# Optimization experiments

Measured on AMD Instinct MI355X. Metric: run time of the kernel, lower is better.

The kernel has to match this reference:

```python
import jax, jax.numpy as jnp
import numpy as np

B, T, V, EMB, KBD, H, NF, OUT = 256, 50, 100000, 64, 64, 128, 10, 64


def setup_inputs() -> dict:
    key = jax.random.key(0)
    ks = jax.random.split(key, 18)
    s = 0.05
    f = lambda i, shape: jax.random.normal(ks[i], shape, jnp.float32) * s
    return {
        "X": jax.random.randint(ks[0], (B, T), 0, V),
        "E": f(1, (V, EMB)),
        "KBE": f(2, (V, KBD)),
        "r_matrix": f(3, (NF, KBD)),
        "gru_Wih": f(4, (3 * H, EMB)),
        "gru_Whh": f(5, (3 * H, H)),
        "gru_bih": f(6, (3 * H,)),
        "gru_bhh": f(7, (3 * H,)),
        "u_W": f(8, (KBD, H)),
        "u_b": f(9, (KBD,)),
        "ea_W": f(10, (KBD, KBD)),
        "ea_b": f(11, (KBD,)),
        "u2_W": f(12, (H, KBD + H)),
        "u2_b": f(13, (H,)),
        "m1_W": f(14, (OUT, H)),
        "m1_b": f(15, (OUT,)),
        "m2_W": f(16, (OUT, EMB + KBD)),
        "m2_b": f(17, (OUT,)),
    }


def reference(X, E, KBE, r_matrix, gru_Wih, gru_Whh, gru_bih, gru_bhh,
              u_W, u_b, ea_W, ea_b, u2_W, u2_b, m1_W, m1_b, m2_W, m2_b):
    b, t = X.shape
    nf, d = r_matrix.shape
    hdim = gru_Whh.shape[1]
    # mask row 0 of the embedding tables (padding item)
    Em = E.at[0].set(0.0)
    KBEm = KBE.at[0].set(0.0)
    Sx = Em[X]        # [B,T,EMB]
    KBx = KBEm[X]     # [B,T,KBD]

    h0 = jnp.zeros((b, hdim), Sx.dtype)
    MN0 = jnp.zeros((b, nf, d), Sx.dtype)
    ysum0 = jnp.zeros((b, m1_b.shape[0]), Sx.dtype)

    def step(carry, xs):
        h, MN, ysum = carry
        x_emb, kb = xs
        # torch GRUCell
        gi = x_emb @ gru_Wih.T + gru_bih
        gh = h @ gru_Whh.T + gru_bhh
        ir, iz, inn = jnp.split(gi, 3, axis=1)
        hr, hz, hn = jnp.split(gh, 3, axis=1)
        r = jax.nn.sigmoid(ir + hr)
        z = jax.nn.sigmoid(iz + hz)
        n = jnp.tanh(inn + r * hn)
        h = (1.0 - z) * n + z * h
        # memory write
        EA = jnp.tanh(kb @ ea_W.T + ea_b)[:, None, :] + r_matrix      # [B,NF,D]
        gate = jax.nn.sigmoid(jnp.sum(MN * EA, axis=-1, keepdims=True))  # [B,NF,1]
        MN = MN * (1.0 - gate) + EA * gate
        # memory read
        U = jnp.tanh(h @ u_W.T + u_b)                                  # [B,D]
        AW = jax.nn.softmax(U @ r_matrix.T, axis=1)                    # [B,NF]
        AC = jnp.einsum('bnd,bn->bd', MN, AW)                          # [B,D]
        Ut = jnp.tanh(jnp.concatenate([h, AC], axis=-1) @ u2_W.T + u2_b)
        y = jnp.tanh(Ut @ m1_W.T + m1_b)                               # [B,OUT]
        return (h, MN, ysum + y), None

    (h, MN, ysum), _ = jax.lax.scan(
        step, (h0, MN0, ysum0),
        (Sx.transpose(1, 0, 2), KBx.transpose(1, 0, 2)))
    y = ysum / t

    MergeE = jnp.concatenate([E, KBE], axis=1).at[0].set(0.0)  # [V, EMB+KBD]
    Sy = jnp.tanh(MergeE @ m2_W.T + m2_b)                      # [V, OUT]
    return jax.nn.log_softmax(y @ Sy.T, axis=1)                # [B, V]
```

## Files before the change

kernel.cpp:

```cpp
#include <hip/hip_runtime.h>
#include <hip/hip_bf16.h>
#include <math.h>

#define BB 256
#define TT 50
#define VV 100000
#define EMB 64
#define KBD 64
#define HH 128
#define NF 10
#define OUTD 64
#define G3H 384
#define NTILE 6250
#define DSTR 16
#define NSY 240
#define TCH 4
#define NUTY (16*13)

typedef __attribute__((ext_vector_type(8))) short sh8;
typedef __attribute__((ext_vector_type(4))) short sh4;
typedef __attribute__((ext_vector_type(4))) float f32x4;

__device__ __forceinline__ float frcp(float x){ return __builtin_amdgcn_rcpf(x); }
__device__ __forceinline__ float sigm(float x){ return frcp(1.0f+__expf(-x)); }
__device__ __forceinline__ float tanhf_(float x){ return 1.0f - 2.0f*frcp(__expf(2.0f*x)+1.0f); }
__device__ __forceinline__ short f2bs(float f){ __hip_bfloat16 h=__float2bfloat16(f); return *reinterpret_cast<short*>(&h); }
__device__ __forceinline__ sh8 ldfrag(const float* p){
  float4 a = *(const float4*)p; float4 b = *(const float4*)(p+4);
  sh8 v;
  v[0]=f2bs(a.x); v[1]=f2bs(a.y); v[2]=f2bs(a.z); v[3]=f2bs(a.w);
  v[4]=f2bs(b.x); v[5]=f2bs(b.y); v[6]=f2bs(b.z); v[7]=f2bs(b.w);
  return v;
}
__device__ __forceinline__ sh8 ldfrag_s(const float* p, float s){
  float4 a = *(const float4*)p; float4 b = *(const float4*)(p+4);
  sh8 v;
  v[0]=f2bs(a.x*s); v[1]=f2bs(a.y*s); v[2]=f2bs(a.z*s); v[3]=f2bs(a.w*s);
  v[4]=f2bs(b.x*s); v[5]=f2bs(b.y*s); v[6]=f2bs(b.z*s); v[7]=f2bs(b.w*s);
  return v;
}
__device__ __forceinline__ void barrier_lds(){
  asm volatile("s_waitcnt lgkmcnt(0)" ::: "memory");
  __builtin_amdgcn_sched_barrier(0);
  __builtin_amdgcn_s_barrier();
  __builtin_amdgcn_sched_barrier(0);
}

#define PREP 32
__global__ __launch_bounds__(512) void k_pre(
    const int* __restrict__ X, const float* __restrict__ E, const float* __restrict__ KBE,
    const float* __restrict__ Wih, const float* __restrict__ bih, const float* __restrict__ bhh,
    const float* __restrict__ eaW, const float* __restrict__ eab,
    float* __restrict__ gi_pre, float* __restrict__ ea_pre,
    __hip_bfloat16* __restrict__ ea_bfT, float* __restrict__ denom,
    float* __restrict__ ybf32,
    const float* __restrict__ m2W, const float* __restrict__ m2b,
    __hip_bfloat16* __restrict__ Sy) {
  const int tid = threadIdx.x;
  const int w = tid>>6, l = tid&63, r16 = l&15, g4 = l>>4;

  if (blockIdx.x >= 400) {
    int kof = g4*8;
    sh8 bbf[4][4];
    float bias[4];
    #pragma unroll
    for (int nt=0;nt<4;nt++){
      int o = nt*16 + r16;
      bias[nt] = m2b[o];
      #pragma unroll
      for (int ks=0;ks<4;ks++) bbf[nt][ks] = ldfrag(m2W + o*128 + ks*32 + kof);
    }
    int wid = (blockIdx.x-400)*8 + w;
    for (int tile=wid; tile<NTILE; tile+=NSY*8){
      int v = tile*16 + r16;
      sh8 aa[4];
      const float* ep = E + (size_t)v*EMB + kof;
      const float* kp = KBE + (size_t)v*KBD + kof;
      aa[0] = ldfrag(ep); aa[1] = ldfrag(ep+32);
      aa[2] = ldfrag(kp); aa[3] = ldfrag(kp+32);
      if (v==0){ sh8 z={0,0,0,0,0,0,0,0}; aa[0]=z;aa[1]=z;aa[2]=z;aa[3]=z; }
      f32x4 acc[4];
      #pragma unroll
      for (int nt=0;nt<4;nt++){ f32x4 z={0.f,0.f,0.f,0.f}; acc[nt]=z; }
      #pragma unroll
      for (int nt=0;nt<4;nt++)
        #pragma unroll
        for (int ks=0;ks<4;ks++)
          acc[nt] = __builtin_amdgcn_mfma_f32_16x16x32_bf16(aa[ks],bbf[nt][ks],acc[nt],0,0,0);
      #pragma unroll
      for (int nt=0;nt<4;nt++){
        #pragma unroll
        for (int r=0;r<4;r++){
          int vv = tile*16 + g4*4 + r;
          Sy[(size_t)vv*OUTD + nt*16 + r16] = __float2bfloat16(tanhf_(acc[nt][r] + bias[nt]));
        }
      }
    }
    return;
  }

  if (blockIdx.x == 0){
    for (int i=tid;i<BB*DSTR;i+=512) denom[i]=0.f;
    for (int i=tid;i<BB*OUTD;i+=512) ybf32[i]=0.f;
  }
  __shared__ float xeL[PREP][68];
  __shared__ float kbL[PREP][68];
  int base = blockIdx.x * PREP;
  for (int i=tid; i<PREP*EMB; i+=512){
    int p=i>>6, k=i&63; int x = X[base+p];
    xeL[p][k] = x ? E[(size_t)x*EMB+k] : 0.0f;
    kbL[p][k] = x ? KBE[(size_t)x*KBD+k] : 0.0f;
  }
  __syncthreads();

  const int m = w>>2, nq = w&3;
  sh8 axe[2], akb[2];
  #pragma unroll
  for (int f=0;f<2;f++){
    axe[f] = ldfrag(&xeL[m*16 + r16][f*32 + g4*8]);
    akb[f] = ldfrag(&kbL[m*16 + r16][f*32 + g4*8]);
  }
  #pragma unroll
  for (int i=0;i<6;i++){
    int nt = nq*6 + i;
    int j = nt*16 + r16;
    sh8 bf0 = ldfrag(Wih + (size_t)j*EMB + g4*8);
    sh8 bf1 = ldfrag(Wih + (size_t)j*EMB + 32 + g4*8);
    f32x4 acc = {0.f,0.f,0.f,0.f};
    acc = __builtin_amdgcn_mfma_f32_16x16x32_bf16(axe[0], bf0, acc,0,0,0);
    acc = __builtin_amdgcn_mfma_f32_16x16x32_bf16(axe[1], bf1, acc,0,0,0);
    float bj = bih[j] + (j < 2*HH ? bhh[j] : 0.0f);
    #pragma unroll
    for (int r=0;r<4;r++){
      int pair = base + m*16 + g4*4 + r;
      gi_pre[(size_t)pair*G3H + j] = acc[r] + bj;
    }
  }
  {
    int d = nq*16 + r16;
    sh8 bf0 = ldfrag(eaW + (size_t)d*KBD + g4*8);
    sh8 bf1 = ldfrag(eaW + (size_t)d*KBD + 32 + g4*8);
    f32x4 acc = {0.f,0.f,0.f,0.f};
    acc = __builtin_amdgcn_mfma_f32_16x16x32_bf16(akb[0], bf0, acc,0,0,0);
    acc = __builtin_amdgcn_mfma_f32_16x16x32_bf16(akb[1], bf1, acc,0,0,0);
    float bd = eab[d];
    #pragma unroll
    for (int r=0;r<4;r++){
      int pair = base + m*16 + g4*4 + r;
      float v = tanhf(acc[r] + bd);
      ea_pre[(size_t)pair*KBD + d] = v;
      int bb = pair/TT, tt = pair - bb*TT;
      ea_bfT[((size_t)bb*64 + d)*64 + tt] = __float2bfloat16(v);
    }
  }
}

__global__ __launch_bounds__(256,2) void k_scanh(
    const float* __restrict__ gi_pre,
    const float* __restrict__ Whh, const float* __restrict__ bhh,
    const float* __restrict__ ea_pre, const float* __restrict__ rmat,
    float* __restrict__ Gg, float* __restrict__ Pg,
    __hip_bfloat16* __restrict__ h_stream) {
  const int tid = threadIdx.x;
  const int w = tid>>6, l = tid&63, r16 = l&15, g4 = l>>4;

  if (blockIdx.x >= 16) {
    const int b = (blockIdx.x-16)*4 + w;
    sh8 aa[4][2];
    #pragma unroll
    for (int i=0;i<4;i++){
      int row = i*16 + r16; if (row > TT-1) row = TT-1;
      #pragma unroll
      for (int f=0;f<2;f++)
        aa[i][f] = ldfrag(ea_pre + ((size_t)b*TT + row)*KBD + f*32 + g4*8);
    }
    sh8 rmB[2];
    #pragma unroll
    for (int f=0;f<2;f++){
      sh8 z = {0,0,0,0,0,0,0,0};
      if (r16 < NF) z = ldfrag(rmat + (size_t)r16*KBD + f*32 + g4*8);
      rmB[f] = z;
    }
    float* Gb = Gg + ((size_t)b<<12);
    #pragma unroll
    for (int i=0;i<4;i++){
      #pragma unroll
      for (int j=0;j<4;j++){
        f32x4 acc={0.f,0.f,0.f,0.f};
        #pragma unroll
        for (int f=0;f<2;f++) acc = __builtin_amdgcn_mfma_f32_16x16x32_bf16(aa[i][f], aa[j][f], acc,0,0,0);
        #pragma unroll
        for (int r=0;r<4;r++) Gb[(i*16+g4*4+r)*64 + j*16+r16] = acc[r];
      }
      f32x4 accp={0.f,0.f,0.f,0.f};
      #pragma unroll
      for (int f=0;f<2;f++) accp = __builtin_amdgcn_mfma_f32_16x16x32_bf16(aa[i][f], rmB[f], accp,0,0,0);
      #pragma unroll
      for (int r=0;r<4;r++) Pg[((size_t)b<<10) + (i*16+g4*4+r)*16 + r16] = accp[r];
    }
    return;
  }

  __shared__ __hip_bfloat16 hcat[2][16][128];
  __builtin_amdgcn_s_setprio(1);
  const int b = blockIdx.x;
  const int b0 = b*16;
  for (int i=tid;i<2*16*128;i+=256) ((short*)hcat)[i]=0;
  __syncthreads();
  const int swz = (r16&7)<<4;

  sh8 whhF[2][3][4];
  #pragma unroll
  for (int t=0;t<2;t++)
    #pragma unroll
    for (int g=0;g<3;g++){
      int chain = (w + 4*t) + 8*g;
      #pragma unroll
      for (int f=0;f<4;f++)
        whhF[t][g][f] = ldfrag(Whh + (size_t)(chain*16 + r16)*HH + f*32 + g4*8);
    }
  float4 bhn[2];
  bhn[0] = *(const float4*)(bhh + 2*HH + w*16 + g4*4);
  bhn[1] = *(const float4*)(bhh + 2*HH + (w+4)*16 + g4*4);
  float h_old[2][4] = {{0.f,0.f,0.f,0.f},{0.f,0.f,0.f,0.f}};
  const float* gi_row = gi_pre + (size_t)(b0+r16)*TT*G3H;
  __hip_bfloat16* hsb = h_stream + (size_t)b*TT*16*HH;

  int cur = 0;
  auto stepfn = [&](int s, float4 (&gi)[2][3], int cu){
    const char* hrow = (const char*)&hcat[cu][r16][0];
    sh8 hb[4];
    #pragma unroll
    for (int f=0;f<4;f++)
      hb[f] = *(const sh8*)(hrow + ((f*64 + g4*16) ^ swz));
    f32x4 aR[2], aZ[2], aN[2];
    #pragma unroll
    for (int t=0;t<2;t++){ f32x4 z={0.f,0.f,0.f,0.f}; aR[t]=z; aZ[t]=z; aN[t]=z; }
    #pragma unroll
    for (int f=0;f<4;f++){
      #pragma unroll
      for (int t=0;t<2;t++){
        aR[t] = __builtin_amdgcn_mfma_f32_16x16x32_bf16(whhF[t][0][f], hb[f], aR[t],0,0,0);
        aZ[t] = __builtin_amdgcn_mfma_f32_16x16x32_bf16(whhF[t][1][f], hb[f], aZ[t],0,0,0);
        aN[t] = __builtin_amdgcn_mfma_f32_16x16x32_bf16(whhF[t][2][f], hb[f], aN[t],0,0,0);
      }
    }
    char* hwrow = (char*)&hcat[cu^1][r16][0];
    #pragma unroll
    for (int t=0;t<2;t++){
      sh4 hp;
      #pragma unroll
      for (int r=0;r<4;r++){
        float rr = sigm(gi[t][0][r] + aR[t][r]);
        float zz = sigm(gi[t][1][r] + aZ[t][r]);
        float nn = tanhf_(gi[t][2][r] + rr*(aN[t][r] + bhn[t][r]));
        h_old[t][r] = (1.f-zz)*nn + zz*h_old[t][r];
        hp[r] = f2bs(h_old[t][r]);
      }
      *(sh4*)(hwrow + (((w+4*t)*32 + g4*8) ^ swz)) = hp;
      *(sh4*)(hsb + ((size_t)s*16 + r16)*HH + (w+4*t)*16 + g4*4) = hp;
    }
    barrier_lds();
  };

  float4 gA[2][3], gB[2][3];
  #pragma unroll
  for (int t=0;t<2;t++)
    #pragma unroll
    for (int g=0;g<3;g++)
      gA[t][g] = *(const float4*)(gi_row + g*128 + (w+4*t)*16 + g4*4);

  for (int s=0;s<TT;s+=2){
    {
      int sg = s+1;
      #pragma unroll
      for (int t=0;t<2;t++)
        #pragma unroll
        for (int g=0;g<3;g++)
          gB[t][g] = *(const float4*)(gi_row + (size_t)sg*G3H + g*128 + (w+4*t)*16 + g4*4);
      stepfn(s, gA, cur);
      cur ^= 1;
    }
    {
      int sg = (s+2<TT)? s+2 : TT-1;
      #pragma unroll
      for (int t=0;t<2;t++)
        #pragma unroll
        for (int g=0;g<3;g++)
          gA[t][g] = *(const float4*)(gi_row + (size_t)sg*G3H + g*128 + (w+4*t)*16 + g4*4);
      stepfn(s+1, gB, cur);
      cur ^= 1;
    }
  }
}

__global__ __launch_bounds__(640) void k_mnac(
    const float* __restrict__ Gg, const float* __restrict__ Pg,
    const float* __restrict__ rmat,
    const __hip_bfloat16* __restrict__ h_stream,
    const float* __restrict__ uW, const float* __restrict__ ub,
    const __hip_bfloat16* __restrict__ ea_bfT,
    __hip_bfloat16* __restrict__ ac_pre) {
  __shared__ __hip_bfloat16 U_sh[64][72];
  __shared__ float aw_sh[64*16];
  __shared__ float AagL[64*52];
  __shared__ float BagL[64*16];
  const int tid = threadIdx.x;
  const int n = tid>>6, l = tid&63, r16 = l&15, g4 = l>>4;
  const int b = blockIdx.x;
  for (int i=tid;i<64*52;i+=640) AagL[i]=0.f;
  for (int i=tid;i<64*16;i+=640) BagL[i]=0.f;

  const __hip_bfloat16* hsb = h_stream + ((size_t)(b>>4)*TT)*16*HH + (size_t)(b&15)*HH;

  #pragma unroll
  for (int cc=0; cc<2; cc++){
    int c = n + cc*10;
    if (c < 16){
      int mi = c>>2, ni = c&3;
      int t = mi*16 + r16; int tt = (t<TT)? t : TT-1;
      sh8 hfr[4], wfr[4];
      #pragma unroll
      for (int f=0;f<4;f++){
        hfr[f] = *(const sh8*)(hsb + (size_t)tt*16*HH + f*32 + g4*8);
        wfr[f] = ldfrag(uW + (size_t)(ni*16+r16)*HH + f*32 + g4*8);
      }
      f32x4 acc = {0.f,0.f,0.f,0.f};
      #pragma unroll
      for (int f=0;f<4;f++)
        acc = __builtin_amdgcn_mfma_f32_16x16x32_bf16(wfr[f], hfr[f], acc,0,0,0);
      float4 ubv = *(const float4*)(ub + ni*16 + g4*4);
      #pragma unroll
      for (int r=0;r<4;r++)
        U_sh[mi*16 + r16][ni*16 + g4*4 + r] = __float2bfloat16(tanhf_(acc[r] + ubv[r]));
    }
  }
  __syncthreads();
  if (n < 4){
    sh8 rmF[2];
    #pragma unroll
    for (int f=0;f<2;f++){
      sh8 z = {0,0,0,0,0,0,0,0};
      if (r16 < NF) z = ldfrag(rmat + (size_t)r16*KBD + f*32 + g4*8);
      rmF[f] = z;
    }
    sh8 uf[2];
    #pragma unroll
    for (int f=0;f<2;f++) uf[f] = *(const sh8*)&U_sh[n*16 + r16][f*32 + g4*8];
    f32x4 al={0.f,0.f,0.f,0.f};
    #pragma unroll
    for (int f=0;f<2;f++) al = __builtin_amdgcn_mfma_f32_16x16x32_bf16(rmF[f], uf[f], al,0,0,0);
    float mx = -1e30f;
    #pragma unroll
    for (int r=0;r<4;r++){ if (g4*4+r < NF) mx = fmaxf(mx, al[r]); }
    mx = fmaxf(mx, __shfl_xor(mx,16));
    mx = fmaxf(mx, __shfl_xor(mx,32));
    float av[4]; float ssum=0.f;
    #pragma unroll
    for (int r=0;r<4;r++){ av[r] = (g4*4+r < NF) ? __expf(al[r]-mx) : 0.f; ssum += av[r]; }
    ssum += __shfl_xor(ssum,16); ssum += __shfl_xor(ssum,32);
    float inv = frcp(ssum);
    #pragma unroll
    for (int r=0;r<4;r++){
      int nn = g4*4+r;
      if (nn < NF) aw_sh[(n*16 + r16)*16 + nn] = av[r]*inv;
    }
  }
  __syncthreads();

  float rv = rmat[n*KBD + l];
  float R = rv*rv;
  R += __shfl_xor(R,1); R += __shfl_xor(R,2); R += __shfl_xor(R,4);
  R += __shfl_xor(R,8); R += __shfl_xor(R,16); R += __shfl_xor(R,32);

  float Pn = (l<TT)? Pg[((size_t)b<<10) + l*16 + n] : 0.f;
  const float* Gb = Gg + ((size_t)b<<12);
  float Grow = Gb[l];
  float d=0.f, w_=0.f, q=1.f;

  for (int t=0;t<TT;t++){
    int tn = (t+1<TT)? t+1 : TT-1;
    float GrowN = Gb[tn*64 + l];
    float dt = __shfl(d, t);
    float g  = sigm(dt);
    float og = 1.f - g;
    float Pt = __shfl(Pn, t);
    float Ets = Grow + Pt + Pn + R;
    d = og*d + g*Ets;
    w_ = (l==t)? g : w_*og;
    q *= og;
    float awt = aw_sh[t*16 + n];
    if (l < TT) atomicAdd(&AagL[t*52 + l], awt*w_);
    if (l == 0) BagL[t*16 + n] = awt*(1.f - q);
    Grow = GrowN;
  }
  __syncthreads();

  if (n < 4){
    const int w = n;
    sh8 a1[4][2], a2[4];
    #pragma unroll
    for (int i=0;i<4;i++){
      int row = i*16 + r16;
      #pragma unroll
      for (int f=0;f<2;f++) a1[i][f] = ldfrag(&AagL[row*52 + f*32 + g4*8]);
      a2[i] = ldfrag(&BagL[row*16 + ((g4*8) & 15)]);
      if (g4 >= 2){ sh8 z={0,0,0,0,0,0,0,0}; a2[i]=z; }
    }
    int j = w;
    sh8 bb1[2];
    #pragma unroll
    for (int f=0;f<2;f++)
      bb1[f] = *(const sh8*)(ea_bfT + ((size_t)b<<12) + (j*16+r16)*64 + f*32 + g4*8);
    sh8 bb2;
    #pragma unroll
    for (int c=0;c<8;c++){
      int k = g4*8 + c;
      bb2[c] = (k<NF)? f2bs(rmat[k*KBD + j*16+r16]) : (short)0;
    }
    #pragma unroll
    for (int i=0;i<4;i++){
      f32x4 acc={0.f,0.f,0.f,0.f};
      #pragma unroll
      for (int f=0;f<2;f++) acc = __builtin_amdgcn_mfma_f32_16x16x32_bf16(a1[i][f], bb1[f], acc,0,0,0);
      acc = __builtin_amdgcn_mfma_f32_16x16x32_bf16(a2[i], bb2, acc,0,0,0);
      #pragma unroll
      for (int r=0;r<4;r++){
        int t = i*16 + g4*4 + r;
        if (t < TT)
          ac_pre[((size_t)t*256 + b)*KBD + j*16 + r16] = __float2bfloat16(acc[r]);
      }
    }
  }
}

__global__ __launch_bounds__(512) void k_uty(
    const __hip_bfloat16* __restrict__ h_stream, const __hip_bfloat16* __restrict__ ac_pre,
    const float* __restrict__ u2W, const float* __restrict__ u2b,
    const float* __restrict__ m1W, const float* __restrict__ m1b,
    float* __restrict__ ybf32) {
  __shared__ __hip_bfloat16 ut_sh[2][16][136];
  const int tid = threadIdx.x;
  const int w = tid>>6, l = tid&63, r16 = l&15, g4 = l>>4;

  const int btile = blockIdx.x & 15, tc = blockIdx.x >> 4;
  const int b0 = btile*16, fb = btile;

  sh8 u2F[6];
  #pragma unroll
  for (int f=0;f<6;f++) u2F[f] = ldfrag(u2W + (size_t)(w*16+r16)*(HH+KBD) + f*32 + g4*8);
  sh8 m1F[4];
  if (w<4){
    #pragma unroll
    for (int f=0;f<4;f++) m1F[f] = ldfrag(m1W + (size_t)(w*16+r16)*HH + f*32 + g4*8);
  }
  float4 u2bv = *(const float4*)(u2b + w*16 + g4*4);
  float4 m1bv = (w<4) ? *(const float4*)(m1b + w*16 + g4*4) : float4{0.f,0.f,0.f,0.f};

  #pragma unroll
  for (int it=0; it<TCH; it++){
    int t = tc*TCH + it;
    if (t >= TT) break;
    const int bu = it & 1;
    const __hip_bfloat16* hp = h_stream + (size_t)((fb*TT + t)*16)*HH;
    const __hip_bfloat16* ap = ac_pre + ((size_t)t*256 + b0)*KBD;
    sh8 cb[6];
    #pragma unroll
    for (int f=0;f<4;f++) cb[f] = *(const sh8*)(hp + r16*HH + f*32 + g4*8);
    #pragma unroll
    for (int f=4;f<6;f++) cb[f] = *(const sh8*)(ap + r16*KBD + (f-4)*32 + g4*8);
    f32x4 at={0.f,0.f,0.f,0.f};
    #pragma unroll
    for (int f=0;f<6;f++) at = __builtin_amdgcn_mfma_f32_16x16x32_bf16(u2F[f], cb[f], at,0,0,0);
    sh4 tp;
    #pragma unroll
    for (int r=0;r<4;r++) tp[r] = f2bs(tanhf_(at[r] + u2bv[r]));
    *(sh4*)&ut_sh[bu][r16][w*16+g4*4] = tp;
    __syncthreads();
    if (w<4){
      sh8 tb[4];
      #pragma unroll
      for (int f=0;f<4;f++) tb[f] = *(const sh8*)&ut_sh[bu][r16][f*32+g4*8];
      f32x4 ay={0.f,0.f,0.f,0.f};
      #pragma unroll
      for (int f=0;f<4;f++) ay = __builtin_amdgcn_mfma_f32_16x16x32_bf16(m1F[f], tb[f], ay,0,0,0);
      #pragma unroll
      for (int r=0;r<4;r++)
        atomicAdd(&ybf32[(size_t)(b0 + r16)*OUTD + w*16 + g4*4 + r], tanhf_(ay[r] + m1bv[r]));
    }
  }
}

__global__ __launch_bounds__(256) void k_logits(
    const float* __restrict__ ybf32, const __hip_bfloat16* __restrict__ Sy,
    float* __restrict__ denom, float* __restrict__ out, int pass) {
  __shared__ float dsum[64];
  int lane = threadIdx.x & 63;
  int w = threadIdx.x >> 6;
  int r16 = lane & 15, g4 = lane >> 4;
  int kof = g4 * 8;
  int tbase = blockIdx.x * 16 + w * 4;
  const float SC = 1.0f/TT;
  if (pass==0){
    if (threadIdx.x<64) dsum[threadIdx.x]=0.f;
    __syncthreads();
  }
  sh8 b0[4], b1[4];
  #pragma unroll
  for (int i=0;i<4;i++){
    if (tbase + i < NTILE) {
      const __hip_bfloat16* bp = Sy + ((size_t)((tbase+i)*16 + r16))*OUTD + kof;
      b0[i] = *(const sh8*)bp;
      b1[i] = *(const sh8*)(bp + 32);
    } else {
      sh8 z = {0,0,0,0,0,0,0,0};
      b0[i]=z; b1[i]=z;
    }
  }
  int bg0 = blockIdx.y * 4;
  for (int bgi=0; bgi<4; bgi++){
    int bg = bg0 + bgi;
    const float* ap = ybf32 + (size_t)(bg*16 + r16)*OUTD + kof;
    sh8 a0 = ldfrag_s(ap, SC);
    sh8 a1 = ldfrag_s(ap+32, SC);
    if (pass == 0){
      float part[4] = {0.f,0.f,0.f,0.f};
      #pragma unroll
      for (int i=0;i<4;i++){
        if (tbase + i < NTILE){
          f32x4 acc = {0.f,0.f,0.f,0.f};
          acc = __builtin_amdgcn_mfma_f32_16x16x32_bf16(a0,b0[i],acc,0,0,0);
          acc = __builtin_amdgcn_mfma_f32_16x16x32_bf16(a1,b1[i],acc,0,0,0);
          #pragma unroll
          for (int r=0;r<4;r++) part[r] += __expf(acc[r]);
        }
      }
      #pragma unroll
      for (int r=0;r<4;r++){
        float p = part[r];
        p += __shfl_xor(p,1,16); p += __shfl_xor(p,2,16);
        p += __shfl_xor(p,4,16); p += __shfl_xor(p,8,16);
        if (r16==0) atomicAdd(&dsum[bgi*16 + g4*4 + r], p);
      }
    } else {
      float lse[4];
      #pragma unroll
      for (int r=0;r<4;r++) lse[r] = logf(denom[(size_t)(bg*16 + g4*4 + r)*DSTR]);
      #pragma unroll
      for (int i=0;i<4;i++){
        if (tbase + i < NTILE){
          f32x4 acc = {0.f,0.f,0.f,0.f};
          acc = __builtin_amdgcn_mfma_f32_16x16x32_bf16(a0,b0[i],acc,0,0,0);
          acc = __builtin_amdgcn_mfma_f32_16x16x32_bf16(a1,b1[i],acc,0,0,0);
          int vc = (tbase+i)*16 + r16;
          #pragma unroll
          for (int r=0;r<4;r++)
            out[(size_t)(bg*16 + g4*4 + r)*VV + vc] = acc[r] - lse[r];
        }
      }
    }
  }
  if (pass==0){
    __syncthreads();
    if (threadIdx.x<64)
      atomicAdd(&denom[(size_t)(bg0*16 + threadIdx.x)*DSTR], dsum[threadIdx.x]);
  }
}

extern "C" void kernel_launch(void* const* d_in, const int* in_sizes, int n_in,
                              void* d_out, int out_size, void* d_ws, size_t ws_size,
                              hipStream_t stream) {
  const int*   X    = (const int*)  d_in[0];
  const float* E    = (const float*)d_in[1];
  const float* KBE  = (const float*)d_in[2];
  const float* rmat = (const float*)d_in[3];
  const float* Wih  = (const float*)d_in[4];
  const float* Whh  = (const float*)d_in[5];
  const float* bih  = (const float*)d_in[6];
  const float* bhh  = (const float*)d_in[7];
  const float* uW   = (const float*)d_in[8];
  const float* ub   = (const float*)d_in[9];
  const float* eaW  = (const float*)d_in[10];
  const float* eab  = (const float*)d_in[11];
  const float* u2W  = (const float*)d_in[12];
  const float* u2b  = (const float*)d_in[13];
  const float* m1W  = (const float*)d_in[14];
  const float* m1b  = (const float*)d_in[15];
  const float* m2W  = (const float*)d_in[16];
  const float* m2b  = (const float*)d_in[17];
  float* outp = (float*)d_out;

  char* p = (char*)d_ws;
  float* gi_pre = (float*)p;            p += (size_t)BB*TT*G3H*4;
  float* ea_pre = (float*)p;            p += (size_t)BB*TT*KBD*4;
  float* denom  = (float*)p;            p += (size_t)BB*DSTR*4;
  float* ybf32  = (float*)p;            p += (size_t)BB*OUTD*4;
  float* Gg     = (float*)p;            p += (size_t)BB*64*64*4;
  float* Pg     = (float*)p;            p += (size_t)BB*64*16*4;
  __hip_bfloat16* h_stream = (__hip_bfloat16*)p; p += (size_t)16*TT*16*HH*2;
  __hip_bfloat16* ea_bfT = (__hip_bfloat16*)p;   p += (size_t)BB*64*64*2;
  __hip_bfloat16* ac_pre = (__hip_bfloat16*)p;   p += (size_t)BB*TT*KBD*2;
  __hip_bfloat16* Sy     = (__hip_bfloat16*)p;   p += (size_t)VV*OUTD*2;

  k_pre<<<400+NSY,512,0,stream>>>(X,E,KBE,Wih,bih,bhh,eaW,eab,gi_pre,ea_pre,ea_bfT,
                                  denom,ybf32,m2W,m2b,Sy);
  k_scanh<<<80,256,0,stream>>>(gi_pre,Whh,bhh,ea_pre,rmat,Gg,Pg,h_stream);
  k_mnac<<<256,640,0,stream>>>(Gg,Pg,rmat,h_stream,uW,ub,ea_bfT,ac_pre);
  k_uty<<<NUTY,512,0,stream>>>(h_stream,ac_pre,u2W,u2b,m1W,m1b,ybf32);
  dim3 g1((NTILE + 15)/16, 4, 1);
  k_logits<<<g1,256,0,stream>>>(ybf32,Sy,denom,outp,0);
  k_logits<<<g1,256,0,stream>>>(ybf32,Sy,denom,outp,1);
}
```

Measured before the change: 224.3 us.

## Fuse Ut/y projection kernel into k_mnac via shared memory

Removes the separate k_uty kernel and the ac_pre global buffer. Each k_mnac block now keeps the AC rows for its batch element in shared memory, computes Ut and y with MFMA, reduces y over time with shuffles, and issues one atomic per output element. This saves a kernel launch and a global round-trip of AC, and cuts the number of atomics. In exchange each block reloads the u2W and m1W fragments from global memory per tile, uses more shared memory, and the phase now runs on only 256 blocks.

```diff
diff --git a/kernel.cpp b/kernel.cpp
--- a/kernel.cpp
+++ b/kernel.cpp
@@ -14,8 +14,6 @@
 #define NTILE 6250
 #define DSTR 16
 #define NSY 240
-#define TCH 4
-#define NUTY (16*13)
 
 typedef __attribute__((ext_vector_type(8))) short sh8;
 typedef __attribute__((ext_vector_type(4))) short sh4;
@@ -299,12 +297,16 @@
     const float* __restrict__ rmat,
     const __hip_bfloat16* __restrict__ h_stream,
     const float* __restrict__ uW, const float* __restrict__ ub,
+    const float* __restrict__ u2W, const float* __restrict__ u2b,
+    const float* __restrict__ m1W, const float* __restrict__ m1b,
     const __hip_bfloat16* __restrict__ ea_bfT,
-    __hip_bfloat16* __restrict__ ac_pre) {
+    float* __restrict__ ybf32) {
   __shared__ __hip_bfloat16 U_sh[64][72];
   __shared__ float aw_sh[64*16];
   __shared__ float AagL[64*52];
   __shared__ float BagL[64*16];
+  __shared__ __hip_bfloat16 ac_sh[64][72];
+  __shared__ __hip_bfloat16 ut_sh[64][136];
   const int tid = threadIdx.x;
   const int n = tid>>6, l = tid&63, r16 = l&15, g4 = l>>4;
   const int b = blockIdx.x;
@@ -397,7 +399,7 @@
   __syncthreads();
 
   if (n < 4){
-    const int w = n;
+    const int jw = n;
     sh8 a1[4][2], a2[4];
     #pragma unroll
     for (int i=0;i<4;i++){
@@ -407,16 +409,15 @@
       a2[i] = ldfrag(&BagL[row*16 + ((g4*8) & 15)]);
       if (g4 >= 2){ sh8 z={0,0,0,0,0,0,0,0}; a2[i]=z; }
     }
-    int j = w;
     sh8 bb1[2];
     #pragma unroll
     for (int f=0;f<2;f++)
-      bb1[f] = *(const sh8*)(ea_bfT + ((size_t)b<<12) + (j*16+r16)*64 + f*32 + g4*8);
+      bb1[f] = *(const sh8*)(ea_bfT + ((size_t)b<<12) + (jw*16+r16)*64 + f*32 + g4*8);
     sh8 bb2;
     #pragma unroll
     for (int c=0;c<8;c++){
       int k = g4*8 + c;
-      bb2[c] = (k<NF)? f2bs(rmat[k*KBD + j*16+r16]) : (short)0;
+      bb2[c] = (k<NF)? f2bs(rmat[k*KBD + jw*16+r16]) : (short)0;
     }
     #pragma unroll
     for (int i=0;i<4;i++){
@@ -427,66 +428,60 @@
       #pragma unroll
       for (int r=0;r<4;r++){
         int t = i*16 + g4*4 + r;
-        if (t < TT)
-          ac_pre[((size_t)t*256 + b)*KBD + j*16 + r16] = __float2bfloat16(acc[r]);
-      }
-    }
-  }
-}
-
-__global__ __launch_bounds__(512) void k_uty(
-    const __hip_bfloat16* __restrict__ h_stream, const __hip_bfloat16* __restrict__ ac_pre,
-    const float* __restrict__ u2W, const float* __restrict__ u2b,
-    const float* __restrict__ m1W, const float* __restrict__ m1b,
-    float* __restrict__ ybf32) {
-  __shared__ __hip_bfloat16 ut_sh[2][16][136];
-  const int tid = threadIdx.x;
-  const int w = tid>>6, l = tid&63, r16 = l&15, g4 = l>>4;
-
-  const int btile = blockIdx.x & 15, tc = blockIdx.x >> 4;
-  const int b0 = btile*16, fb = btile;
-
-  sh8 u2F[6];
-  #pragma unroll
-  for (int f=0;f<6;f++) u2F[f] = ldfrag(u2W + (size_t)(w*16+r16)*(HH+KBD) + f*32 + g4*8);
-  sh8 m1F[4];
-  if (w<4){
-    #pragma unroll
-    for (int f=0;f<4;f++) m1F[f] = ldfrag(m1W + (size_t)(w*16+r16)*HH + f*32 + g4*8);
-  }
-  float4 u2bv = *(const float4*)(u2b + w*16 + g4*4);
-  float4 m1bv = (w<4) ? *(const float4*)(m1b + w*16 + g4*4) : float4{0.f,0.f,0.f,0.f};
-
-  #pragma unroll
-  for (int it=0; it<TCH; it++){
-    int t = tc*TCH + it;
-    if (t >= TT) break;
-    const int bu = it & 1;
-    const __hip_bfloat16* hp = h_stream + (size_t)((fb*TT + t)*16)*HH;
-    const __hip_bfloat16* ap = ac_pre + ((size_t)t*256 + b0)*KBD;
-    sh8 cb[6];
-    #pragma unroll
-    for (int f=0;f<4;f++) cb[f] = *(const sh8*)(hp + r16*HH + f*32 + g4*8);
-    #pragma unroll
-    for (int f=4;f<6;f++) cb[f] = *(const sh8*)(ap + r16*KBD + (f-4)*32 + g4*8);
-    f32x4 at={0.f,0.f,0.f,0.f};
-    #pragma unroll
-    for (int f=0;f<6;f++) at = __builtin_amdgcn_mfma_f32_16x16x32_bf16(u2F[f], cb[f], at,0,0,0);
-    sh4 tp;
-    #pragma unroll
-    for (int r=0;r<4;r++) tp[r] = f2bs(tanhf_(at[r] + u2bv[r]));
-    *(sh4*)&ut_sh[bu][r16][w*16+g4*4] = tp;
-    __syncthreads();
-    if (w<4){
-      sh8 tb[4];
-      #pragma unroll
-      for (int f=0;f<4;f++) tb[f] = *(const sh8*)&ut_sh[bu][r16][f*32+g4*8];
-      f32x4 ay={0.f,0.f,0.f,0.f};
-      #pragma unroll
-      for (int f=0;f<4;f++) ay = __builtin_amdgcn_mfma_f32_16x16x32_bf16(m1F[f], tb[f], ay,0,0,0);
+        ac_sh[t][jw*16 + r16] = __float2bfloat16(acc[r]);
+      }
+    }
+  }
+  __syncthreads();
+
+  #pragma unroll
+  for (int cc=0; cc<4; cc++){
+    int c = n + cc*10;
+    if (c < 32){
+      int mi = c>>3, ni = c&7;
+      int t = mi*16 + r16; int tt = (t<TT)? t : TT-1;
+      sh8 cb[6], wf[6];
+      #pragma unroll
+      for (int f=0;f<4;f++) cb[f] = *(const sh8*)(hsb + (size_t)tt*16*HH + f*32 + g4*8);
+      #pragma unroll
+      for (int f=4;f<6;f++) cb[f] = *(const sh8*)&ac_sh[t][(f-4)*32 + g4*8];
+      #pragma unroll
+      for (int f=0;f<6;f++) wf[f] = ldfrag(u2W + (size_t)(ni*16+r16)*(HH+KBD) + f*32 + g4*8);
+      f32x4 at = {0.f,0.f,0.f,0.f};
+      #pragma unroll
+      for (int f=0;f<6;f++) at = __builtin_amdgcn_mfma_f32_16x16x32_bf16(wf[f], cb[f], at,0,0,0);
+      float4 u2bv = *(const float4*)(u2b + ni*16 + g4*4);
       #pragma unroll
       for (int r=0;r<4;r++)
-        atomicAdd(&ybf32[(size_t)(b0 + r16)*OUTD + w*16 + g4*4 + r], tanhf_(ay[r] + m1bv[r]));
+        ut_sh[mi*16 + r16][ni*16 + g4*4 + r] = __float2bfloat16(tanhf_(at[r] + u2bv[r]));
+    }
+  }
+  __syncthreads();
+
+  #pragma unroll
+  for (int cc=0; cc<2; cc++){
+    int c = n + cc*10;
+    if (c < 16){
+      int mi = c>>2, ni = c&3;
+      sh8 tb[4], mf[4];
+      #pragma unroll
+      for (int f=0;f<4;f++){
+        tb[f] = *(const sh8*)&ut_sh[mi*16 + r16][f*32 + g4*8];
+        mf[f] = ldfrag(m1W + (size_t)(ni*16+r16)*HH + f*32 + g4*8);
+      }
+      f32x4 ay = {0.f,0.f,0.f,0.f};
+      #pragma unroll
+      for (int f=0;f<4;f++) ay = __builtin_amdgcn_mfma_f32_16x16x32_bf16(mf[f], tb[f], ay,0,0,0);
+      float4 m1bv = *(const float4*)(m1b + ni*16 + g4*4);
+      int t = mi*16 + r16;
+      #pragma unroll
+      for (int r=0;r<4;r++){
+        float val = (t < TT) ? tanhf_(ay[r] + m1bv[r]) : 0.f;
+        val += __shfl_xor(val,1); val += __shfl_xor(val,2);
+        val += __shfl_xor(val,4); val += __shfl_xor(val,8);
+        if (r16 == 0)
+          atomicAdd(&ybf32[(size_t)b*OUTD + ni*16 + g4*4 + r], val);
+      }
     }
   }
 }
@@ -599,14 +594,12 @@
   float* Pg     = (float*)p;            p += (size_t)BB*64*16*4;
   __hip_bfloat16* h_stream = (__hip_bfloat16*)p; p += (size_t)16*TT*16*HH*2;
   __hip_bfloat16* ea_bfT = (__hip_bfloat16*)p;   p += (size_t)BB*64*64*2;
-  __hip_bfloat16* ac_pre = (__hip_bfloat16*)p;   p += (size_t)BB*TT*KBD*2;
   __hip_bfloat16* Sy     = (__hip_bfloat16*)p;   p += (size_t)VV*OUTD*2;
 
   k_pre<<<400+NSY,512,0,stream>>>(X,E,KBE,Wih,bih,bhh,eaW,eab,gi_pre,ea_pre,ea_bfT,
                                   denom,ybf32,m2W,m2b,Sy);
   k_scanh<<<80,256,0,stream>>>(gi_pre,Whh,bhh,ea_pre,rmat,Gg,Pg,h_stream);
-  k_mnac<<<256,640,0,stream>>>(Gg,Pg,rmat,h_stream,uW,ub,ea_bfT,ac_pre);
-  k_uty<<<NUTY,512,0,stream>>>(h_stream,ac_pre,u2W,u2b,m1W,m1b,ybf32);
+  k_mnac<<<256,640,0,stream>>>(Gg,Pg,rmat,h_stream,uW,ub,u2W,u2b,m1W,m1b,ea_bfT,ybf32);
   dim3 g1((NTILE + 15)/16, 4, 1);
   k_logits<<<g1,256,0,stream>>>(ybf32,Sy,denom,outp,0);
   k_logits<<<g1,256,0,stream>>>(ybf32,Sy,denom,outp,1);
```

Result: no change. 224.1 us (-0.1%).
